# Optimization experiments

Measured on AMD Instinct MI355X. Metric: run time of the kernel, lower is better.

## Reference

```python
import jax, jax.numpy as jnp
import numpy as np

# dims (see shape_source)
B, S, DM, H, CIN, COUT, E = 4, 1024, 256, 8, 23, 256, 16
D2 = 2 * DM                                  # MoE dim = cat(attn_out, queries)
HE = int(D2 * 4 * 2 / 3)                     # geglu/expert hidden = 1365
CAP = max(4, min(S, int(S * 2.0 / E)))       # eval capacity_factor=2.0 -> 128
THRESH = 0.2                                 # threshold_eval for 2nd expert
BAL_COEF, Z_COEF = 0.01, 0.001


def _gelu(x):
    return jax.nn.gelu(x, approximate=False)  # torch nn.GELU default = erf


def _layernorm(x, g, b, eps=1e-5):
    m = x.mean(-1, keepdims=True)
    v = ((x - m) ** 2).mean(-1, keepdims=True)
    return (x - m) * jax.lax.rsqrt(v + eps) * g + b


def _rmsnorm(x, g):
    # st-moe RMSNorm: F.normalize(x) * sqrt(d) * gamma
    n = jnp.sqrt((x * x).sum(-1, keepdims=True))
    return x / jnp.maximum(n, 1e-12) * jnp.float32(np.sqrt(x.shape[-1])) * g


def _geglu_ff(x, g, w1, b1, mult, w2, b2):
    # st-moe Expert with prenorm=True: RMSNorm -> Linear -> GEGLU -> Linear
    h = _rmsnorm(x, g) @ w1 + b1
    a, gate = jnp.split(h, 2, axis=-1)
    return (_gelu(gate) * a * mult) @ w2 + b2


def _mha(q_in, k_in, v_in, wq, bq, wk, bk, wv, bv, wo, bo):
    b, sq, d = q_in.shape
    hd = d // H
    def heads(t):
        return t.reshape(b, -1, H, hd).transpose(0, 2, 1, 3)  # (b,H,s,hd)
    q = heads(q_in @ wq + bq)
    k = heads(k_in @ wk + bk)
    v = heads(v_in @ wv + bv)
    scale = jnp.float32(1.0 / np.sqrt(hd))
    att = jax.nn.softmax(jnp.einsum('bhqd,bhkd->bhqk', q, k) * scale, axis=-1)
    o = jnp.einsum('bhqk,bhkd->bhqd', att, v).transpose(0, 2, 1, 3).reshape(b, sq, d)
    return o @ wo + bo


def _moe(x, gate_w, ln_g, ln_b, w1, b1, w2, b2):
    # top-2 gating with threshold + capacity, dense dispatch/combine (eval semantics)
    logits = jnp.einsum('bnd,ed->bne', x, gate_w)
    raw = jax.nn.softmax(logits, axis=-1)
    gates2, idx2 = jax.lax.top_k(raw, 2)                       # (b,n,2)
    gates2 = gates2 / jnp.maximum(gates2.sum(-1, keepdims=True), 1e-9)
    g1, g2 = gates2[..., 0], gates2[..., 1]
    route2 = (g2 > THRESH).astype(x.dtype)
    oh1 = jax.nn.one_hot(idx2[..., 0], E, dtype=x.dtype)       # (b,n,e)
    oh2 = jax.nn.one_hot(idx2[..., 1], E, dtype=x.dtype) * route2[..., None]
    pos1 = jnp.cumsum(oh1, axis=1) - oh1                       # slot within expert
    pos2 = jnp.cumsum(oh2, axis=1) - oh2 + oh1.sum(axis=1, keepdims=True)
    keep1 = oh1 * (pos1 < CAP).astype(x.dtype)
    keep2 = oh2 * (pos2 < CAP).astype(x.dtype)
    capoh1 = jax.nn.one_hot(jnp.clip(pos1, 0, CAP - 1).astype(jnp.int32), CAP, dtype=x.dtype)
    capoh2 = jax.nn.one_hot(jnp.clip(pos2, 0, CAP - 1).astype(jnp.int32), CAP, dtype=x.dtype)
    combine = (g1[..., None, None] * keep1[..., None] * capoh1
               + g2[..., None, None] * keep2[..., None] * capoh2)  # (b,n,e,c)
    dispatch = (combine > 0).astype(x.dtype)
    xin = jnp.einsum('bnec,bnd->ebcd', dispatch, x)            # (e,b,c,d)
    # Expert_alt: LayerNorm -> Linear -> LeakyReLU -> Linear, vectorized over experts
    h = _layernorm(xin, ln_g[:, None, None, :], ln_b[:, None, None, :])
    h = jax.nn.leaky_relu(jnp.einsum('ebcd,edh->ebch', h, w1) + b1[:, None, None, :])
    h = jnp.einsum('ebch,ehd->ebcd', h, w2) + b2[:, None, None, :]
    out = jnp.einsum('bnec,ebcd->bnd', combine, h)
    balance = (raw.mean(axis=1) * oh1.mean(axis=1)).mean() * jnp.float32(E * E) * BAL_COEF
    z = (jax.nn.logsumexp(logits, axis=-1) ** 2).mean() * Z_COEF
    return out, balance + z, balance, z


def setup_inputs() -> dict:
    key = jax.random.key(0)
    ks = iter(jax.random.split(key, 64))
    f32 = jnp.float32
    def rn(shape, std=0.02):
        return jax.random.normal(next(ks), shape, dtype=f32) * std
    return {
        'K': jax.random.normal(next(ks), (B, S, 3), dtype=f32),
        'V': jax.random.normal(next(ks), (B, S, CIN), dtype=f32),
        'Q': jax.random.normal(next(ks), (B, S, 3), dtype=f32),
        'w_topo': rn((3, DM)), 'b_topo': jnp.zeros((DM,), f32),
        'w_val': rn((CIN, DM)), 'b_val': jnp.zeros((DM,), f32),
        'wq': rn((DM, DM)), 'bq': jnp.zeros((DM,), f32),
        'wk': rn((DM, DM)), 'bk': jnp.zeros((DM,), f32),
        'wv': rn((DM, DM)), 'bv': jnp.zeros((DM,), f32),
        'wo': rn((DM, DM)), 'bo': jnp.zeros((DM,), f32),
        'ffb_g': jnp.ones((D2,), f32), 'ffb_w1': rn((D2, 2 * HE)),
        'ffb_b1': jnp.zeros((2 * HE,), f32), 'ffb_mult': jnp.ones((HE,), f32),
        'ffb_w2': rn((HE, D2)), 'ffb_b2': jnp.zeros((D2,), f32),
        'prenorm_g': jnp.ones((D2,), f32),
        'gate_w': rn((E, D2)),
        'exp_ln_g': jnp.ones((E, D2), f32), 'exp_ln_b': jnp.zeros((E, D2), f32),
        'exp_w1': rn((E, D2, HE)), 'exp_b1': jnp.zeros((E, HE), f32),
        'exp_w2': rn((E, HE, D2)), 'exp_b2': jnp.zeros((E, D2), f32),
        'ffa_g': jnp.ones((D2,), f32), 'ffa_w1': rn((D2, 2 * HE)),
        'ffa_b1': jnp.zeros((2 * HE,), f32), 'ffa_mult': jnp.ones((HE,), f32),
        'ffa_w2': rn((HE, D2)), 'ffa_b2': jnp.zeros((D2,), f32),
        'w_out': rn((D2, COUT)), 'b_out': jnp.zeros((COUT,), f32),
    }


def reference(K, V, Q, w_topo, b_topo, w_val, b_val, wq, bq, wk, bk, wv, bv, wo, bo,
              ffb_g, ffb_w1, ffb_b1, ffb_mult, ffb_w2, ffb_b2, prenorm_g, gate_w,
              exp_ln_g, exp_ln_b, exp_w1, exp_b1, exp_w2, exp_b2,
              ffa_g, ffa_w1, ffa_b1, ffa_mult, ffa_w2, ffa_b2, w_out, b_out):
    sk = K.shape[1]
    topo = _gelu(jnp.concatenate([K, Q], axis=1) @ w_topo + b_topo)
    keys, queries = topo[:, :sk], topo[:, sk:]
    values = _gelu(V @ w_val + b_val)
    attn = _mha(queries, keys, values, wq, bq, wk, bk, wv, bv, wo, bo)
    x = jnp.concatenate([attn, queries], axis=-1)      # (B, S, D2)
    # SparseMoEBlock with add_ff_before/add_ff_after = True (STMoE_prenorm)
    x = _geglu_ff(x, ffb_g, ffb_w1, ffb_b1, ffb_mult, ffb_w2, ffb_b2) + x
    moe_out, total_aux, bal, z = _moe(_rmsnorm(x, prenorm_g), gate_w,
                                      exp_ln_g, exp_ln_b, exp_w1, exp_b1, exp_w2, exp_b2)
    x = moe_out + x
    x = _geglu_ff(x, ffa_g, ffa_w1, ffa_b1, ffa_mult, ffa_w2, ffa_b2) + x
    out = _gelu(x @ w_out + b_out)
    return out, total_aux, bal, z
```

## Files before the change

kernel.cpp:

```cpp
#include <hip/hip_runtime.h>
#include <hip/hip_bf16.h>
#include <math.h>

#define CAPN 128

typedef short short8 __attribute__((ext_vector_type(8)));
typedef short short4v __attribute__((ext_vector_type(4)));
typedef float f32x4 __attribute__((ext_vector_type(4)));

__device__ __forceinline__ float gelu_f(float x){
  return 0.5f*x*(1.0f+erff(x*0.7071067811865476f));
}
__device__ __forceinline__ void split2(float v, __hip_bfloat16& h, __hip_bfloat16& l){
  h = __float2bfloat16(v);
  l = __float2bfloat16(v - __bfloat162float(h));
}
__device__ __forceinline__ void split2s(float v, short& h, short& l){
  __hip_bfloat16 hh = __float2bfloat16(v);
  __hip_bfloat16 ll = __float2bfloat16(v - __bfloat162float(hh));
  h = *(short*)&hh; l = *(short*)&ll;
}

__global__ __launch_bounds__(256) void topo_kernel(
    const float* __restrict__ K, const float* __restrict__ Q,
    const float* __restrict__ w, const float* __restrict__ b,
    __hip_bfloat16* __restrict__ khi, __hip_bfloat16* __restrict__ klo,
    __hip_bfloat16* __restrict__ qhi, __hip_bfloat16* __restrict__ qlo,
    float* __restrict__ qf32)
{
  int idx = blockIdx.x*256 + threadIdx.x;
  int d = idx & 255;
  int r = idx >> 8;
  int bb = r >> 11;
  int n  = r & 2047;
  const float* src = (n < 1024) ? (K + ((bb<<10) + n)*3)
                                : (Q + ((bb<<10) + (n-1024))*3);
  float v = b[d] + src[0]*w[d] + src[1]*w[256+d] + src[2]*w[512+d];
  v = gelu_f(v);
  int off = (((bb<<10) + (n & 1023))<<8) + d;
  __hip_bfloat16 h, l; split2(v, h, l);
  if (n < 1024){ khi[off] = h; klo[off] = l; }
  else         { qhi[off] = h; qlo[off] = l; qf32[off] = v; }
}

__global__ __launch_bounds__(256) void values_kernel(
    const float* __restrict__ V, const float* __restrict__ w,
    const float* __restrict__ b,
    __hip_bfloat16* __restrict__ vhi, __hip_bfloat16* __restrict__ vlo)
{
  int idx = blockIdx.x*256 + threadIdx.x;
  int d = idx & 255; int r = idx >> 8;
  const float* src = V + r*23;
  float acc = b[d];
  #pragma unroll
  for (int c=0;c<23;c++) acc += src[c]*w[c*256+d];
  acc = gelu_f(acc);
  __hip_bfloat16 h, l; split2(acc, h, l);
  vhi[idx] = h; vlo[idx] = l;
}

#define SLP 40
__global__ __launch_bounds__(256) void sgemm_kernel(
    const __hip_bfloat16* __restrict__ Ah_, const __hip_bfloat16* __restrict__ Al_,
    int lda, long sA,
    const __hip_bfloat16* __restrict__ Wh_, const __hip_bfloat16* __restrict__ Wl_,
    int ldw, long sW,
    const float* __restrict__ bias, int nbias, int bsplit, int bsplitPad, long sB,
    const float* __restrict__ R, int ldr,
    float* __restrict__ C, int ldc, long sC,
    int K, int act,
    float* __restrict__ P, long pz, int splitK)
{
  int z = blockIdx.z / splitK;
  int kc = blockIdx.z - z*splitK;
  const short* Ah = (const short*)Ah_ + (long)z*sA;
  const short* Al = (const short*)Al_ + (long)z*sA;
  const short* Wh = (const short*)Wh_ + (long)z*sW;
  const short* Wl = (const short*)Wl_ + (long)z*sW;
  int bm = blockIdx.y*128, bn = blockIdx.x*128;
  int tid = threadIdx.x, lane = tid & 63, wave = tid >> 6;
  int wm = (wave & 1)*64, wn = (wave >> 1)*64;

  __shared__ short AsH[128*SLP], AsL[128*SLP], BsH[128*SLP], BsL[128*SLP];

  f32x4 acc[4][4];
  f32x4 zero4 = {0.f,0.f,0.f,0.f};
  #pragma unroll
  for (int i=0;i<4;i++)
    #pragma unroll
    for (int j=0;j<4;j++) acc[i][j] = zero4;

  int srow = tid >> 1, scol = (tid & 1)*16;
  int ml = lane & 15, q = lane >> 4;
  long abase = (long)(bm+srow)*lda + scol;
  long bbase = (long)(bn+srow)*ldw + scol;

  int Kc = K / splitK;
  int kbeg = kc * Kc, kend = kbeg + Kc;

  short8 ah0 = *(const short8*)&Ah[abase + kbeg];
  short8 ah1 = *(const short8*)&Ah[abase + kbeg + 8];
  short8 al0 = *(const short8*)&Al[abase + kbeg];
  short8 al1 = *(const short8*)&Al[abase + kbeg + 8];
  short8 bh0 = *(const short8*)&Wh[bbase + kbeg];
  short8 bh1 = *(const short8*)&Wh[bbase + kbeg + 8];
  short8 bl0 = *(const short8*)&Wl[bbase + kbeg];
  short8 bl1 = *(const short8*)&Wl[bbase + kbeg + 8];

  for (int k0 = kbeg; k0 < kend; k0 += 32){
    __syncthreads();
    *(short8*)&AsH[srow*SLP + scol]     = ah0;
    *(short8*)&AsH[srow*SLP + scol + 8] = ah1;
    *(short8*)&AsL[srow*SLP + scol]     = al0;
    *(short8*)&AsL[srow*SLP + scol + 8] = al1;
    *(short8*)&BsH[srow*SLP + scol]     = bh0;
    *(short8*)&BsH[srow*SLP + scol + 8] = bh1;
    *(short8*)&BsL[srow*SLP + scol]     = bl0;
    *(short8*)&BsL[srow*SLP + scol + 8] = bl1;
    __syncthreads();
    if (k0 + 32 < kend){
      long ab = abase + k0 + 32;
      long bb2 = bbase + k0 + 32;
      ah0 = *(const short8*)&Ah[ab];
      ah1 = *(const short8*)&Ah[ab + 8];
      al0 = *(const short8*)&Al[ab];
      al1 = *(const short8*)&Al[ab + 8];
      bh0 = *(const short8*)&Wh[bb2];
      bh1 = *(const short8*)&Wh[bb2 + 8];
      bl0 = *(const short8*)&Wl[bb2];
      bl1 = *(const short8*)&Wl[bb2 + 8];
    }
    short8 afh[4], afl[4], bfh[4], bfl[4];
    #pragma unroll
    for (int i=0;i<4;i++){
      afh[i] = *(const short8*)&AsH[(wm + 16*i + ml)*SLP + q*8];
      afl[i] = *(const short8*)&AsL[(wm + 16*i + ml)*SLP + q*8];
    }
    #pragma unroll
    for (int j=0;j<4;j++){
      bfh[j] = *(const short8*)&BsH[(wn + 16*j + ml)*SLP + q*8];
      bfl[j] = *(const short8*)&BsL[(wn + 16*j + ml)*SLP + q*8];
    }
    #pragma unroll
    for (int i=0;i<4;i++)
      #pragma unroll
      for (int j=0;j<4;j++){
        acc[i][j] = __builtin_amdgcn_mfma_f32_16x16x32_bf16(afh[i], bfh[j], acc[i][j], 0,0,0);
        acc[i][j] = __builtin_amdgcn_mfma_f32_16x16x32_bf16(afh[i], bfl[j], acc[i][j], 0,0,0);
        acc[i][j] = __builtin_amdgcn_mfma_f32_16x16x32_bf16(afl[i], bfh[j], acc[i][j], 0,0,0);
      }
  }

  if (P){
    float* Pb = P + (long)blockIdx.z * pz;
    #pragma unroll
    for (int i=0;i<4;i++)
      #pragma unroll
      for (int r=0;r<4;r++){
        int gm = bm + wm + 16*i + q*4 + r;
        #pragma unroll
        for (int j=0;j<4;j++){
          int gn = bn + wn + 16*j + ml;
          Pb[(long)gm*ldc + gn] = acc[i][j][r];
        }
      }
    return;
  }

  const float* biasz = bias ? bias + (long)z*sB : nullptr;
  long coff = (long)z*sC;
  #pragma unroll
  for (int i=0;i<4;i++){
    #pragma unroll
    for (int r=0;r<4;r++){
      int gm = bm + wm + 16*i + q*4 + r;
      #pragma unroll
      for (int j=0;j<4;j++){
        int gn = bn + wn + 16*j + ml;
        float v = acc[i][j][r];
        if (biasz){
          int bi;
          if (bsplit){
            if (gn < bsplit) bi = gn;
            else if (gn >= bsplitPad && gn < bsplitPad + (nbias - bsplit)) bi = gn - (bsplitPad - bsplit);
            else bi = -1;
          } else bi = (gn < nbias) ? gn : -1;
          if (bi >= 0) v += biasz[bi];
        }
        if (act == 1) v = gelu_f(v);
        if (R) v += R[(long)gm*ldr + gn];
        C[coff + (long)gm*ldc + gn] = v;
      }
    }
  }
}

#define LP 56
__global__ __launch_bounds__(256) void bgemm_kernel(
    const __hip_bfloat16* __restrict__ A, int lda, long sA,
    const __hip_bfloat16* __restrict__ WT, int ldw, long sW,
    const float* __restrict__ bias, int nbias, int bsplit, int bsplitPad, long sB,
    const float* __restrict__ R, int ldr, long sR,
    void* __restrict__ C, int ldc, long sC, int cIsBf16,
    int K, int act,
    float* __restrict__ P, long pz, int splitK)
{
  int z = blockIdx.z / splitK;
  int kc = blockIdx.z - z*splitK;
  const short* Ab = (const short*)A + (long)z*sA;
  const short* Bb = (const short*)WT + (long)z*sW;
  int bm = blockIdx.y*128, bn = blockIdx.x*128;
  int tid = threadIdx.x, lane = tid & 63, wave = tid >> 6;
  int wm = (wave & 1)*64, wn = (wave >> 1)*64;

  __shared__ short As[128*LP];
  __shared__ short Bs[128*LP];

  f32x4 acc[4][4];
  f32x4 zero4 = {0.f,0.f,0.f,0.f};
  #pragma unroll
  for (int i=0;i<4;i++)
    #pragma unroll
    for (int j=0;j<4;j++) acc[i][j] = zero4;

  int g0 = tid, g1 = tid + 256;
  int r0 = g0 >> 2, c0 = (g0 & 3) * 8;
  int r1 = g1 >> 2, c1 = (g1 & 3) * 8;
  int ml = lane & 15, q = lane >> 4;
  long a0base = (long)(bm+r0)*lda + c0;
  long a1base = (long)(bm+r1)*lda + c1;
  long b0base = (long)(bn+r0)*ldw + c0;
  long b1base = (long)(bn+r1)*ldw + c1;

  int Kc = K / splitK;
  int kbeg = kc * Kc, kend = kbeg + Kc;

  short8 av0 = *(const short8*)&Ab[a0base + kbeg];
  short8 av1 = *(const short8*)&Ab[a1base + kbeg];
  short8 bv0 = *(const short8*)&Bb[b0base + kbeg];
  short8 bv1 = *(const short8*)&Bb[b1base + kbeg];

  for (int k0 = kbeg; k0 < kend; k0 += 32){
    __syncthreads();
    *(short8*)&As[r0*LP + c0] = av0;
    *(short8*)&As[r1*LP + c1] = av1;
    *(short8*)&Bs[r0*LP + c0] = bv0;
    *(short8*)&Bs[r1*LP + c1] = bv1;
    __syncthreads();
    if (k0 + 32 < kend){
      av0 = *(const short8*)&Ab[a0base + k0 + 32];
      av1 = *(const short8*)&Ab[a1base + k0 + 32];
      bv0 = *(const short8*)&Bb[b0base + k0 + 32];
      bv1 = *(const short8*)&Bb[b1base + k0 + 32];
    }
    short8 af[4], bfv[4];
    #pragma unroll
    for (int i=0;i<4;i++) af[i]  = *(const short8*)&As[(wm + 16*i + ml)*LP + q*8];
    #pragma unroll
    for (int j=0;j<4;j++) bfv[j] = *(const short8*)&Bs[(wn + 16*j + ml)*LP + q*8];
    #pragma unroll
    for (int i=0;i<4;i++)
      #pragma unroll
      for (int j=0;j<4;j++)
        acc[i][j] = __builtin_amdgcn_mfma_f32_16x16x32_bf16(af[i], bfv[j], acc[i][j], 0,0,0);
  }

  if (P){
    float* Pb = P + (long)blockIdx.z * pz;
    #pragma unroll
    for (int i=0;i<4;i++)
      #pragma unroll
      for (int r=0;r<4;r++){
        int gm = bm + wm + 16*i + q*4 + r;
        #pragma unroll
        for (int j=0;j<4;j++){
          int gn = bn + wn + 16*j + ml;
          Pb[(long)gm*ldc + gn] = acc[i][j][r];
        }
      }
    return;
  }

  const float* biasz = bias ? bias + (long)z*sB : nullptr;
  const float* Rz = R ? R + (long)z*sR : nullptr;
  long coff = (long)z*sC;
  #pragma unroll
  for (int i=0;i<4;i++){
    #pragma unroll
    for (int r=0;r<4;r++){
      int gm = bm + wm + 16*i + q*4 + r;
      #pragma unroll
      for (int j=0;j<4;j++){
        int gn = bn + wn + 16*j + ml;
        float v = acc[i][j][r];
        if (biasz){
          int bi;
          if (bsplit){
            if (gn < bsplit) bi = gn;
            else if (gn >= bsplitPad && gn < bsplitPad + (nbias - bsplit)) bi = gn - (bsplitPad - bsplit);
            else bi = -1;
          } else bi = (gn < nbias) ? gn : -1;
          if (bi >= 0) v += biasz[bi];
        }
        if (act == 2) v = (v > 0.f) ? v : 0.01f*v;
        if (Rz) v += Rz[(long)gm*ldr + gn];
        if (cIsBf16) ((__hip_bfloat16*)C)[coff + (long)gm*ldc + gn] = __float2bfloat16(v);
        else         ((float*)C)[coff + (long)gm*ldc + gn] = v;
      }
    }
  }
}

__global__ __launch_bounds__(256) void reduce_kernel(
    const float* __restrict__ P, long zStride, int nsplit,
    const float* __restrict__ bias,
    const float* __restrict__ R, float* __restrict__ out,
    int Nmask, int logN, int ldOut, int act, long total)
{
  long idx = (long)blockIdx.x*256 + threadIdx.x;
  if (idx >= total) return;
  long zz = idx / zStride;
  long rem = idx - zz*zStride;
  const float* Pb = P + zz*(long)nsplit*zStride + rem;
  float v = 0.f;
  for (int k=0;k<nsplit;k++) v += Pb[(long)k*zStride];
// ... 49 lines not shown
  __shared__ float lds[64][65];
  #pragma unroll
  for (int i=0;i<16;i++){
    int e = tid + i*256;
    int kl = e >> 6, c = e & 63;
    int np = n0 + c;
    int ns;
    if (split){
      if (np < split) ns = np;
      else if (np >= splitPad && np < splitPad + (N - split)) ns = np - (splitPad - split);
      else ns = -1;
    } else ns = (np < N) ? np : -1;
    int k = k0 + kl;
    float v = (ns >= 0 && k < K) ? W[(long)k*N + ns] : 0.f;
    lds[kl][c] = v;
  }
  __syncthreads();
  #pragma unroll
  for (int i=0;i<16;i++){
    int e = tid + i*256;
    int nl = e >> 6, kl = e & 63;
    float v = lds[kl][nl];
    __hip_bfloat16 h, l; split2(v, h, l);
    long o = (long)(n0+nl)*Kpad + k0 + kl;
    outh[o] = h; outl[o] = l;
  }
}

__global__ void pack_bias_kernel(const float* bq, const float* bk, const float* bv, float* out){
  int i = blockIdx.x*256 + threadIdx.x;
  if (i < 256) out[i] = bq[i];
  else if (i < 512) out[i] = bk[i-256];
  else if (i < 768) out[i] = bv[i-512];
}

__global__ __launch_bounds__(256) void qksplit_kernel(
    const float* __restrict__ QP,
    __hip_bfloat16* __restrict__ qsh, __hip_bfloat16* __restrict__ qsl,
    __hip_bfloat16* __restrict__ ksh, __hip_bfloat16* __restrict__ ksl)
{
  int idx = blockIdx.x*256 + threadIdx.x;
  float qv = QP[idx] * 0.17677669529663687f;
  __hip_bfloat16 h, l;
  split2(qv, h, l); qsh[idx] = h; qsl[idx] = l;
  float kv = QP[1048576 + idx];
  split2(kv, h, l); ksh[idx] = h; ksl[idx] = l;
}

__global__ __launch_bounds__(256) void vtrans_kernel(
    const float* __restrict__ VP,
    __hip_bfloat16* __restrict__ vth, __hip_bfloat16* __restrict__ vtl)
{
  int bh = blockIdx.y, bb = bh >> 3, h = bh & 7;
  int s0 = blockIdx.x*64;
  int tid = threadIdx.x;
  __shared__ float t[64][33];
  #pragma unroll
  for (int p=0;p<8;p++){
    int sl = (tid>>5) + p*8;
    int d = tid & 31;
    t[sl][d] = VP[((bb<<10)+s0+sl)*256 + h*32 + d];
  }
  __syncthreads();
  #pragma unroll
  for (int p=0;p<8;p++){
    int dl = (tid>>6) + p*4;
    int s = tid & 63;
    float v = t[s][dl];
    __hip_bfloat16 hh, ll; split2(v, hh, ll);
    vth[(bh*32+dl)*1024 + s0 + s] = hh;
    vtl[(bh*32+dl)*1024 + s0 + s] = ll;
  }
}

#define KSP 40
__global__ __launch_bounds__(256) void attn_mfma_kernel(
    const __hip_bfloat16* __restrict__ qsh_, const __hip_bfloat16* __restrict__ qsl_,
    const __hip_bfloat16* __restrict__ ksh_, const __hip_bfloat16* __restrict__ ksl_,
    const __hip_bfloat16* __restrict__ vth_, const __hip_bfloat16* __restrict__ vtl_,
// ... 64 lines not shown
      split2s(p1, sh, sl2);
      Phw[ml*KSP + 16 + quad*4 + r] = sh;  Plw[ml*KSP + 16 + quad*4 + r] = sl2;
    }
    #pragma unroll
    for (int r=0;r<4;r++){
      float ar = __shfl(alpha, quad*4 + r, 16);
      O0[r] *= ar; O1[r] *= ar; Lacc[r] *= ar;
    }
    short8 pAh = *(const short8*)&Phw[ml*KSP + quad*8];
    short8 pAl = *(const short8*)&Plw[ml*KSP + quad*8];
    short8 vb0h = *(const short8*)&VhS[ml*KSP + quad*8];
    short8 vb0l = *(const short8*)&VlS[ml*KSP + quad*8];
    short8 vb1h = *(const short8*)&VhS[(16+ml)*KSP + quad*8];
    short8 vb1l = *(const short8*)&VlS[(16+ml)*KSP + quad*8];
    O0 = __builtin_amdgcn_mfma_f32_16x16x32_bf16(pAl, vb0h, O0, 0,0,0);
    O0 = __builtin_amdgcn_mfma_f32_16x16x32_bf16(pAh, vb0l, O0, 0,0,0);
    O0 = __builtin_amdgcn_mfma_f32_16x16x32_bf16(pAh, vb0h, O0, 0,0,0);
    O1 = __builtin_amdgcn_mfma_f32_16x16x32_bf16(pAl, vb1h, O1, 0,0,0);
    O1 = __builtin_amdgcn_mfma_f32_16x16x32_bf16(pAh, vb1l, O1, 0,0,0);
    O1 = __builtin_amdgcn_mfma_f32_16x16x32_bf16(pAh, vb1h, O1, 0,0,0);
    Lacc = __builtin_amdgcn_mfma_f32_16x16x32_bf16(pAh, ones, Lacc, 0,0,0);
    Lacc = __builtin_amdgcn_mfma_f32_16x16x32_bf16(pAl, ones, Lacc, 0,0,0);
  }
  #pragma unroll
  for (int r=0;r<4;r++){
    float inv = 1.f / Lacc[r];
    int row = (bb<<10) + q0 + quad*4 + r;
    __hip_bfloat16 hh, ll;
    split2(O0[r]*inv, hh, ll);
    aoh[row*256 + h*32 + ml] = hh;       aol[row*256 + h*32 + ml] = ll;
    split2(O1[r]*inv, hh, ll);
    aoh[row*256 + h*32 + 16 + ml] = hh;  aol[row*256 + h*32 + 16 + ml] = ll;
  }
}

__global__ __launch_bounds__(256) void concat_kernel(
    const float* __restrict__ queries, float* __restrict__ x)
{
  int idx = blockIdx.x*256 + threadIdx.x;
  int d = idx & 255; int r = idx >> 8;
  x[(r<<9) + 256 + d] = queries[idx];
}

__global__ __launch_bounds__(256) void rmsnorm_kernel(
    const float* __restrict__ x, const float* __restrict__ g, float* __restrict__ y)
{
  int r = blockIdx.x; int tid = threadIdx.x;
  float v0 = x[(r<<9) + tid];
  float v1 = x[(r<<9) + 256 + tid];
  float ss = v0*v0 + v1*v1;
  #pragma unroll
  for (int off=32; off>0; off>>=1) ss += __shfl_down(ss, off, 64);
  __shared__ float wsum[4];
  if ((tid & 63) == 0) wsum[tid>>6] = ss;
  __syncthreads();
  float tot = wsum[0]+wsum[1]+wsum[2]+wsum[3];
  float scale = 22.62741699796952f / fmaxf(sqrtf(tot), 1e-12f);
  y[(r<<9) + tid]       = v0*scale*g[tid];
  y[(r<<9) + 256 + tid] = v1*scale*g[256+tid];
}

__global__ __launch_bounds__(256) void rmsnorm_split_kernel(
    const float* __restrict__ x, const float* __restrict__ g,
    __hip_bfloat16* __restrict__ yh, __hip_bfloat16* __restrict__ yl)
{
  int r = blockIdx.x; int tid = threadIdx.x;
  float v0 = x[(r<<9) + tid];
  float v1 = x[(r<<9) + 256 + tid];
  float ss = v0*v0 + v1*v1;
  #pragma unroll
  for (int off=32; off>0; off>>=1) ss += __shfl_down(ss, off, 64);
  __shared__ float wsum[4];
  if ((tid & 63) == 0) wsum[tid>>6] = ss;
  __syncthreads();
// ... 275 lines not shown
  const float* gate_w = (const float*)d_in[22];
  const float* exp_ln_g=(const float*)d_in[23];
  const float* exp_ln_b=(const float*)d_in[24];
  const float* exp_w1 = (const float*)d_in[25];
  const float* exp_b1 = (const float*)d_in[26];
  const float* exp_w2 = (const float*)d_in[27];
  const float* exp_b2 = (const float*)d_in[28];
  const float* ffa_g  = (const float*)d_in[29];
  const float* ffa_w1 = (const float*)d_in[30];
  const float* ffa_b1 = (const float*)d_in[31];
  const float* ffa_mult=(const float*)d_in[32];
  const float* ffa_w2 = (const float*)d_in[33];
  const float* ffa_b2 = (const float*)d_in[34];
  const float* w_out  = (const float*)d_in[35];
  const float* b_out  = (const float*)d_in[36];
  float* dout = (float*)d_out;

  float* wsf = (float*)d_ws;
  int*   wsi = (int*)d_ws;

  const size_t A0 = 0;
  const size_t B0 = 11534336;
  const size_t OXA = 17301504;
  const size_t OXB = 19398656;
  const size_t OWP = 21495808;
  const size_t OMI = 21889024;

  __hip_bfloat16* qhi = (__hip_bfloat16*)(wsf + A0);
  __hip_bfloat16* khi = (__hip_bfloat16*)(wsf + A0 + 524288);
  __hip_bfloat16* vhi = (__hip_bfloat16*)(wsf + A0 + 1048576);
  __hip_bfloat16* qlo = (__hip_bfloat16*)(wsf + A0 + 1572864);
  __hip_bfloat16* klo = (__hip_bfloat16*)(wsf + A0 + 2097152);
  __hip_bfloat16* vlo = (__hip_bfloat16*)(wsf + A0 + 2621440);
  float* QP = wsf + A0 + 3145728;
  __hip_bfloat16* aohi = (__hip_bfloat16*)(wsf + A0 + 6291456);
  __hip_bfloat16* aolo = (__hip_bfloat16*)(wsf + A0 + 6815744);
  __hip_bfloat16* qsh = (__hip_bfloat16*)(wsf + A0);
  __hip_bfloat16* qsl = (__hip_bfloat16*)(wsf + A0 + 524288);
  __hip_bfloat16* ksh = (__hip_bfloat16*)(wsf + A0 + 1048576);
  __hip_bfloat16* ksl = (__hip_bfloat16*)(wsf + A0 + 1572864);
  __hip_bfloat16* vth = (__hip_bfloat16*)(wsf + A0 + 2097152);
  __hip_bfloat16* vtl = (__hip_bfloat16*)(wsf + A0 + 2621440);
  float* QF = wsf + B0 + 262144;
  float* Hb = wsf + A0;
  __hip_bfloat16* yh   = (__hip_bfloat16*)(wsf + B0);
  __hip_bfloat16* yl   = (__hip_bfloat16*)(wsf + B0 + 1048576);
  __hip_bfloat16* fw1h = (__hip_bfloat16*)(wsf + B0 + 2097152);
  __hip_bfloat16* fw1l = fw1h + 1441792;
  __hip_bfloat16* th   = (__hip_bfloat16*)(wsf + B0);
  __hip_bfloat16* tl   = (__hip_bfloat16*)(wsf + B0 + 2883584);
  __hip_bfloat16* fw2h = (__hip_bfloat16*)(wsf + A0);
  __hip_bfloat16* fw2l = fw2h + 720896;
  float* Pffb = wsf + A0 + 1048576;
  __hip_bfloat16* wte   = (__hip_bfloat16*)(wsf + A0);
  __hip_bfloat16* xin_bf= (__hip_bfloat16*)(wsf + A0 + 5767168);
  __hip_bfloat16* h1_bf = (__hip_bfloat16*)(wsf + A0 + 7864320);
  float* H2 = wsf + 13631488;
  float* YM = wsf + B0;
  __hip_bfloat16* y_bf = (__hip_bfloat16*)(wsf + A0);
  __hip_bfloat16* wf1  = (__hip_bfloat16*)(wsf + A0 + 1048576);
  __hip_bfloat16* h_bf = (__hip_bfloat16*)(wsf + A0 + 1769472);
  __hip_bfloat16* t_bf = (__hip_bfloat16*)(wsf + A0 + 7536640);
  __hip_bfloat16* wf2  = (__hip_bfloat16*)(wsf + A0 + 10420224);
  float* Pffa = wsf + B0;
  __hip_bfloat16* xah = (__hip_bfloat16*)(wsf + A0);
  __hip_bfloat16* xal = (__hip_bfloat16*)(wsf + A0 + 1048576);
  float* Pout = wsf + A0 + 2097152;
  __hip_bfloat16* wp = (__hip_bfloat16*)(wsf + OWP);
  __hip_bfloat16* wqh = wp;            __hip_bfloat16* wkh = wp + 65536;
  __hip_bfloat16* wvh = wp + 131072;   __hip_bfloat16* wql = wp + 196608;
  __hip_bfloat16* wkl = wp + 262144;   __hip_bfloat16* wvl = wp + 327680;
  __hip_bfloat16* woh = wp + 393216;   __hip_bfloat16* wol = wp + 458752;
  __hip_bfloat16* wouth = wp + 524288; __hip_bfloat16* woutl = wp + 655360;

  int* idx1 = wsi + OMI + 0;
  int* idx2 = wsi + OMI + 4096;
  int* route= wsi + OMI + 8192;
  int* ts1  = wsi + OMI + 12288;
  int* ts2  = wsi + OMI + 16384;
  int* slot_token = wsi + OMI + 20480;
  int* count1     = wsi + OMI + 28672;
  float* gg1      = wsf + OMI + 28864;
  float* gg2      = wsf + OMI + 32960;
  float* bias_qkv = wsf + OMI + 37056;
  float* rawp     = wsf + OMI + 37824;
  float* lse2     = wsf + OMI + 103360;

  convT2_kernel<<<dim3(4,4),  256, 0, stream>>>(wq, 256, 256, wqh, wql, 256, 256, 0, 0);
  convT2_kernel<<<dim3(4,4),  256, 0, stream>>>(wk, 256, 256, wkh, wkl, 256, 256, 0, 0);
  convT2_kernel<<<dim3(4,4),  256, 0, stream>>>(wv, 256, 256, wvh, wvl, 256, 256, 0, 0);
  convT2_kernel<<<dim3(4,4),  256, 0, stream>>>(wo, 256, 256, woh, wol, 256, 256, 0, 0);
  convT2_kernel<<<dim3(4,8),  256, 0, stream>>>(w_out, 256, 512, wouth, woutl, 256, 512, 0, 0);
  convT2_kernel<<<dim3(44,8), 256, 0, stream>>>(ffb_w1, 2730, 512, fw1h, fw1l, 2816, 512, 1365, 1408);
  pack_bias_kernel<<<3, 256, 0, stream>>>(bq, bk, bv, bias_qkv);

  topo_kernel<<<8192, 256, 0, stream>>>(K_in, Q_in, w_topo, b_topo, khi, klo, qhi, qlo, QF);
  values_kernel<<<4096, 256, 0, stream>>>(V_in, w_val, b_val, vhi, vlo);

  sgemm_kernel<<<dim3(2,32,3), 256, 0, stream>>>(
      qhi, qlo, 256, 1048576, wqh, wql, 256, 65536,
      bias_qkv, 256, 0, 0, 256, nullptr, 0, QP, 256, 1048576, 256, 0,
      nullptr, 0, 1);

  qksplit_kernel<<<4096, 256, 0, stream>>>(QP, qsh, qsl, ksh, ksl);
  vtrans_kernel<<<dim3(16,32), 256, 0, stream>>>(QP + 2097152, vth, vtl);
  attn_mfma_kernel<<<dim3(16,32), 256, 0, stream>>>(qsh, qsl, ksh, ksl, vth, vtl, aohi, aolo);

  sgemm_kernel<<<dim3(2,32,1), 256, 0, stream>>>(
      aohi, aolo, 256, 0, woh, wol, 256, 0,
      bo, 256, 0, 0, 0, nullptr, 0, wsf+OXA, 512, 0, 256, 0,
      nullptr, 0, 1);
  concat_kernel<<<4096, 256, 0, stream>>>(QF, wsf+OXA);

  rmsnorm_split_kernel<<<4096, 256, 0, stream>>>(wsf+OXA, ffb_g, yh, yl);
  sgemm_kernel<<<dim3(22,32,1), 256, 0, stream>>>(
      yh, yl, 512, 0, fw1h, fw1l, 512, 0,
      ffb_b1, 2730, 1365, 1408, 0, nullptr, 0, Hb, 2816, 0, 512, 0,
      nullptr, 0, 1);
  glu_split_kernel<<<22528, 256, 0, stream>>>(Hb, ffb_mult, th, tl);
  convT2_kernel<<<dim3(8,22), 256, 0, stream>>>(ffb_w2, 512, 1365, fw2h, fw2l, 512, 1408, 0, 0);
  sgemm_kernel<<<dim3(4,32,4), 256, 0, stream>>>(
      th, tl, 1408, 0, fw2h, fw2l, 1408, 0,
      nullptr, 0, 0, 0, 0, nullptr, 0, nullptr, 512, 0, 1408, 0,
      Pffb, 2097152, 4);
  reduce_kernel<<<8192, 256, 0, stream>>>(
      Pffb, 2097152, 4, ffb_b2, wsf+OXA, wsf+OXB, 511, 9, 512, 0, 2097152);

  rmsnorm_kernel<<<4096, 256, 0, stream>>>(wsf+OXB, prenorm_g, YM);
  gating_kernel<<<4096, 256, 0, stream>>>(YM, gate_w, idx1, idx2, route, gg1, gg2, rawp, lse2);
  scan_kernel<<<64, 256, 0, stream>>>(idx1, idx2, route, ts1, ts2, slot_token, count1);
  gather_ln_kernel<<<8192, 256, 0, stream>>>(YM, slot_token, exp_ln_g, exp_ln_b, xin_bf);
  convT_kernel<<<dim3(22, 8, 16), 256, 0, stream>>>(exp_w1, 1365, 512, (long)512*1365,
                                                    wte, 1408, 512, (long)1408*512, 0, 0);
  bgemm_kernel<<<dim3(11,4,16), 256, 0, stream>>>(
      xin_bf, 512, (long)512*512, wte, 512, (long)1408*512,
      exp_b1, 1365, 0, 0, 1365, nullptr, 0, 0,
      h1_bf, 1408, (long)512*1408, 1, 512, 2,
      nullptr, 0, 1);
  convT_kernel<<<dim3(8, 22, 16), 256, 0, stream>>>(exp_w2, 512, 1365, (long)1365*512,
                                                    wte, 512, 1408, (long)512*1408, 0, 0);
  bgemm_kernel<<<dim3(4,4,16), 256, 0, stream>>>(
      h1_bf, 1408, (long)512*1408, wte, 1408, (long)512*1408,
      exp_b2, 512, 0, 0, 512, nullptr, 0, 0,
      H2, 512, (long)512*512, 0, 1408, 0,
      nullptr, 0, 1);
  combine_kernel<<<8192, 256, 0, stream>>>(wsf+OXB, H2, ts1, ts2, gg1, gg2);
  aux_kernel<<<1, 256, 0, stream>>>(rawp, lse2, count1, dout + 4096*256);

  rmsnorm_bf_kernel<<<4096, 256, 0, stream>>>(wsf+OXB, ffa_g, y_bf);
  convT_kernel<<<dim3(44, 8, 1), 256, 0, stream>>>(ffa_w1, 2730, 512, 0,
                                                   wf1, 2816, 512, 0, 1365, 1408);
  bgemm_kernel<<<dim3(22,32,1), 256, 0, stream>>>(
      y_bf, 512, 0, wf1, 512, 0,
      ffa_b1, 2730, 1365, 1408, 0, nullptr, 0, 0,
      h_bf, 2816, 0, 1, 512, 0,
      nullptr, 0, 1);
  glu_bf_kernel<<<22528, 256, 0, stream>>>(h_bf, ffa_mult, t_bf);
  convT_kernel<<<dim3(8, 22, 1), 256, 0, stream>>>(ffa_w2, 512, 1365, 0,
                                                   wf2, 512, 1408, 0, 0, 0);
  bgemm_kernel<<<dim3(4,32,2), 256, 0, stream>>>(
      t_bf, 1408, 0, wf2, 1408, 0,
      nullptr, 0, 0, 0, 0, nullptr, 0, 0,
      nullptr, 512, 0, 0, 1408, 0,
      Pffa, 2097152, 2);
  reduce_kernel<<<8192, 256, 0, stream>>>(
      Pffa, 2097152, 2, ffa_b2, wsf+OXB, wsf+OXA, 511, 9, 512, 0, 2097152);

  split32_kernel<<<8192, 256, 0, stream>>>(wsf+OXA, xah, xal);
  sgemm_kernel<<<dim3(2,32,4), 256, 0, stream>>>(
      xah, xal, 512, 0, wouth, woutl, 512, 0,
      nullptr, 0, 0, 0, 0, nullptr, 0, nullptr, 256, 0, 512, 0,
      Pout, 1048576, 4);
  reduce_kernel<<<4096, 256, 0, stream>>>(
      Pout, 1048576, 4, b_out, nullptr, dout, 255, 8, 256, 1, 1048576);
}
```

Baseline: 804.8 us.

## Halve GEMM N-tile to 64 and fuse QK split and concat into producers

Both split-bf16 and plain bf16 GEMM kernels shrink their N tile from 128 to 64, with per-wave 64x32 sub-tiles and doubled grid widths, to raise block count and occupancy on the small GEMMs. The QKV projection epilogue now scales Q and writes hi/lo bf16 splits for Q and K directly, which removes the separate qksplit kernel. The topo kernel writes the queries straight into the concatenated x buffer, which removes the concat kernel. The smaller tiles lower per-block operand reuse and add more global loads per FLOP.

New measurement: 808.9 us. About the same (+0.5%).

```diff
diff --git a/kernel.cpp b/kernel.cpp
--- a/kernel.cpp
+++ b/kernel.cpp
@@ -26,7 +26,7 @@
     const float* __restrict__ w, const float* __restrict__ b,
     __hip_bfloat16* __restrict__ khi, __hip_bfloat16* __restrict__ klo,
     __hip_bfloat16* __restrict__ qhi, __hip_bfloat16* __restrict__ qlo,
-    float* __restrict__ qf32)
+    float* __restrict__ xa)
 {
   int idx = blockIdx.x*256 + threadIdx.x;
   int d = idx & 255;
@@ -37,10 +37,13 @@
                                 : (Q + ((bb<<10) + (n-1024))*3);
   float v = b[d] + src[0]*w[d] + src[1]*w[256+d] + src[2]*w[512+d];
   v = gelu_f(v);
-  int off = (((bb<<10) + (n & 1023))<<8) + d;
+  int tok = (bb<<10) + (n & 1023);
   __hip_bfloat16 h, l; split2(v, h, l);
-  if (n < 1024){ khi[off] = h; klo[off] = l; }
-  else         { qhi[off] = h; qlo[off] = l; qf32[off] = v; }
+  if (n < 1024){ khi[(tok<<8)+d] = h; klo[(tok<<8)+d] = l; }
+  else {
+    qhi[(tok<<8)+d] = h; qlo[(tok<<8)+d] = l;
+    xa[(tok<<9) + 256 + d] = v;
+  }
 }
 
 __global__ __launch_bounds__(256) void values_kernel(
@@ -69,7 +72,9 @@
     const float* __restrict__ R, int ldr,
     float* __restrict__ C, int ldc, long sC,
     int K, int act,
-    float* __restrict__ P, long pz, int splitK)
+    float* __restrict__ P, long pz, int splitK,
+    __hip_bfloat16* __restrict__ APh, __hip_bfloat16* __restrict__ APl,
+    long APz, int attnPrep)
 {
   int z = blockIdx.z / splitK;
   int kc = blockIdx.z - z*splitK;
@@ -77,23 +82,22 @@
   const short* Al = (const short*)Al_ + (long)z*sA;
   const short* Wh = (const short*)Wh_ + (long)z*sW;
   const short* Wl = (const short*)Wl_ + (long)z*sW;
-  int bm = blockIdx.y*128, bn = blockIdx.x*128;
+  int bm = blockIdx.y*128, bn = blockIdx.x*64;
   int tid = threadIdx.x, lane = tid & 63, wave = tid >> 6;
-  int wm = (wave & 1)*64, wn = (wave >> 1)*64;
-
-  __shared__ short AsH[128*SLP], AsL[128*SLP], BsH[128*SLP], BsL[128*SLP];
-
-  f32x4 acc[4][4];
+  int wm = (wave & 1)*64, wn = (wave >> 1)*32;
+
+  __shared__ short AsH[128*SLP], AsL[128*SLP], BsH[64*SLP], BsL[64*SLP];
+
+  f32x4 acc[4][2];
   f32x4 zero4 = {0.f,0.f,0.f,0.f};
   #pragma unroll
-  for (int i=0;i<4;i++)
-    #pragma unroll
-    for (int j=0;j<4;j++) acc[i][j] = zero4;
-
-  int srow = tid >> 1, scol = (tid & 1)*16;
+  for (int i=0;i<4;i++){ acc[i][0] = zero4; acc[i][1] = zero4; }
+
+  int arow = tid >> 1, acol = (tid & 1)*16;
+  int brow = tid >> 2, bcol = (tid & 3)*8;
   int ml = lane & 15, q = lane >> 4;
-  long abase = (long)(bm+srow)*lda + scol;
-  long bbase = (long)(bn+srow)*ldw + scol;
+  long abase = (long)(bm+arow)*lda + acol;
+  long bbase = (long)(bn+brow)*ldw + bcol;
 
   int Kc = K / splitK;
   int kbeg = kc * Kc, kend = kbeg + Kc;
@@ -103,20 +107,16 @@
   short8 al0 = *(const short8*)&Al[abase + kbeg];
   short8 al1 = *(const short8*)&Al[abase + kbeg + 8];
   short8 bh0 = *(const short8*)&Wh[bbase + kbeg];
-  short8 bh1 = *(const short8*)&Wh[bbase + kbeg + 8];
   short8 bl0 = *(const short8*)&Wl[bbase + kbeg];
-  short8 bl1 = *(const short8*)&Wl[bbase + kbeg + 8];
 
   for (int k0 = kbeg; k0 < kend; k0 += 32){
     __syncthreads();
-    *(short8*)&AsH[srow*SLP + scol]     = ah0;
-    *(short8*)&AsH[srow*SLP + scol + 8] = ah1;
-    *(short8*)&AsL[srow*SLP + scol]     = al0;
-    *(short8*)&AsL[srow*SLP + scol + 8] = al1;
-    *(short8*)&BsH[srow*SLP + scol]     = bh0;
-    *(short8*)&BsH[srow*SLP + scol + 8] = bh1;
-    *(short8*)&BsL[srow*SLP + scol]     = bl0;
-    *(short8*)&BsL[srow*SLP + scol + 8] = bl1;
+    *(short8*)&AsH[arow*SLP + acol]     = ah0;
+    *(short8*)&AsH[arow*SLP + acol + 8] = ah1;
+    *(short8*)&AsL[arow*SLP + acol]     = al0;
+    *(short8*)&AsL[arow*SLP + acol + 8] = al1;
+    *(short8*)&BsH[brow*SLP + bcol]     = bh0;
+    *(short8*)&BsL[brow*SLP + bcol]     = bl0;
     __syncthreads();
     if (k0 + 32 < kend){
       long ab = abase + k0 + 32;
@@ -126,25 +126,23 @@
       al0 = *(const short8*)&Al[ab];
       al1 = *(const short8*)&Al[ab + 8];
       bh0 = *(const short8*)&Wh[bb2];
-      bh1 = *(const short8*)&Wh[bb2 + 8];
       bl0 = *(const short8*)&Wl[bb2];
-      bl1 = *(const short8*)&Wl[bb2 + 8];
     }
-    short8 afh[4], afl[4], bfh[4], bfl[4];
+    short8 afh[4], afl[4], bfh[2], bfl[2];
     #pragma unroll
     for (int i=0;i<4;i++){
       afh[i] = *(const short8*)&AsH[(wm + 16*i + ml)*SLP + q*8];
       afl[i] = *(const short8*)&AsL[(wm + 16*i + ml)*SLP + q*8];
     }
     #pragma unroll
-    for (int j=0;j<4;j++){
+    for (int j=0;j<2;j++){
       bfh[j] = *(const short8*)&BsH[(wn + 16*j + ml)*SLP + q*8];
       bfl[j] = *(const short8*)&BsL[(wn + 16*j + ml)*SLP + q*8];
     }
     #pragma unroll
     for (int i=0;i<4;i++)
       #pragma unroll
-      for (int j=0;j<4;j++){
+      for (int j=0;j<2;j++){
         acc[i][j] = __builtin_amdgcn_mfma_f32_16x16x32_bf16(afh[i], bfh[j], acc[i][j], 0,0,0);
         acc[i][j] = __builtin_amdgcn_mfma_f32_16x16x32_bf16(afh[i], bfl[j], acc[i][j], 0,0,0);
         acc[i][j] = __builtin_amdgcn_mfma_f32_16x16x32_bf16(afl[i], bfh[j], acc[i][j], 0,0,0);
@@ -159,7 +157,7 @@
       for (int r=0;r<4;r++){
         int gm = bm + wm + 16*i + q*4 + r;
         #pragma unroll
-        for (int j=0;j<4;j++){
+        for (int j=0;j<2;j++){
           int gn = bn + wn + 16*j + ml;
           Pb[(long)gm*ldc + gn] = acc[i][j][r];
         }
@@ -175,7 +173,7 @@
     for (int r=0;r<4;r++){
       int gm = bm + wm + 16*i + q*4 + r;
       #pragma unroll
-      for (int j=0;j<4;j++){
+      for (int j=0;j<2;j++){
         int gn = bn + wn + 16*j + ml;
         float v = acc[i][j][r];
         if (biasz){
@@ -187,6 +185,17 @@
           } else bi = (gn < nbias) ? gn : -1;
           if (bi >= 0) v += biasz[bi];
         }
+        if (attnPrep){
+          if (z < 2){
+            if (z == 0) v *= 0.17677669529663687f;
+            __hip_bfloat16 hh, ll; split2(v, hh, ll);
+            APh[(long)z*APz + (long)gm*256 + gn] = hh;
+            APl[(long)z*APz + (long)gm*256 + gn] = ll;
+          } else {
+            C[(long)gm*ldc + gn] = v;
+          }
+          continue;
+        }
         if (act == 1) v = gelu_f(v);
         if (R) v += R[(long)gm*ldr + gn];
         C[coff + (long)gm*ldc + gn] = v;
@@ -195,7 +204,7 @@
   }
 }
 
-#define LP 56
+#define LP 40
 __global__ __launch_bounds__(256) void bgemm_kernel(
     const __hip_bfloat16* __restrict__ A, int lda, long sA,
     const __hip_bfloat16* __restrict__ WT, int ldw, long sW,
@@ -209,59 +218,51 @@
   int kc = blockIdx.z - z*splitK;
   const short* Ab = (const short*)A + (long)z*sA;
   const short* Bb = (const short*)WT + (long)z*sW;
-  int bm = blockIdx.y*128, bn = blockIdx.x*128;
+  int bm = blockIdx.y*128, bn = blockIdx.x*64;
   int tid = threadIdx.x, lane = tid & 63, wave = tid >> 6;
-  int wm = (wave & 1)*64, wn = (wave >> 1)*64;
+  int wm = (wave & 1)*64, wn = (wave >> 1)*32;
 
   __shared__ short As[128*LP];
-  __shared__ short Bs[128*LP];
-
-  f32x4 acc[4][4];
+  __shared__ short Bs[64*LP];
+
+  f32x4 acc[4][2];
   f32x4 zero4 = {0.f,0.f,0.f,0.f};
   #pragma unroll
-  for (int i=0;i<4;i++)
-    #pragma unroll
-    for (int j=0;j<4;j++) acc[i][j] = zero4;
-
-  int g0 = tid, g1 = tid + 256;
-  int r0 = g0 >> 2, c0 = (g0 & 3) * 8;
-  int r1 = g1 >> 2, c1 = (g1 & 3) * 8;
+  for (int i=0;i<4;i++){ acc[i][0] = zero4; acc[i][1] = zero4; }
+
+  int arow = tid >> 1, acol = (tid & 1)*16;
+  int brow = tid >> 2, bcol = (tid & 3)*8;
   int ml = lane & 15, q = lane >> 4;
-  long a0base = (long)(bm+r0)*lda + c0;
-  long a1base = (long)(bm+r1)*lda + c1;
-  long b0base = (long)(bn+r0)*ldw + c0;
-  long b1base = (long)(bn+r1)*ldw + c1;
+  long abase = (long)(bm+arow)*lda + acol;
+  long bbase = (long)(bn+brow)*ldw + bcol;
 
   int Kc = K / splitK;
   int kbeg = kc * Kc, kend = kbeg + Kc;
 
-  short8 av0 = *(const short8*)&Ab[a0base + kbeg];
-  short8 av1 = *(const short8*)&Ab[a1base + kbeg];
-  short8 bv0 = *(const short8*)&Bb[b0base + kbeg];
-  short8 bv1 = *(const short8*)&Bb[b1base + kbeg];
+  short8 av0 = *(const short8*)&Ab[abase + kbeg];
+  short8 av1 = *(const short8*)&Ab[abase + kbeg + 8];
+  short8 bv0 = *(const short8*)&Bb[bbase + kbeg];
 
   for (int k0 = kbeg; k0 < kend; k0 += 32){
     __syncthreads();
-    *(short8*)&As[r0*LP + c0] = av0;
-    *(short8*)&As[r1*LP + c1] = av1;
-    *(short8*)&Bs[r0*LP + c0] = bv0;
-    *(short8*)&Bs[r1*LP + c1] = bv1;
+    *(short8*)&As[arow*LP + acol]     = av0;
+    *(short8*)&As[arow*LP + acol + 8] = av1;
+    *(short8*)&Bs[brow*LP + bcol]     = bv0;
     __syncthreads();
     if (k0 + 32 < kend){
-      av0 = *(const short8*)&Ab[a0base + k0 + 32];
-      av1 = *(const short8*)&Ab[a1base + k0 + 32];
-      bv0 = *(const short8*)&Bb[b0base + k0 + 32];
-      bv1 = *(const short8*)&Bb[b1base + k0 + 32];
+      av0 = *(const short8*)&Ab[abase + k0 + 32];
+      av1 = *(const short8*)&Ab[abase + k0 + 40];
+      bv0 = *(const short8*)&Bb[bbase + k0 + 32];
     }
-    short8 af[4], bfv[4];
+    short8 af[4], bfv[2];
     #pragma unroll
     for (int i=0;i<4;i++) af[i]  = *(const short8*)&As[(wm + 16*i + ml)*LP + q*8];
     #pragma unroll
-    for (int j=0;j<4;j++) bfv[j] = *(const short8*)&Bs[(wn + 16*j + ml)*LP + q*8];
+    for (int j=0;j<2;j++) bfv[j] = *(const short8*)&Bs[(wn + 16*j + ml)*LP + q*8];
     #pragma unroll
     for (int i=0;i<4;i++)
       #pragma unroll
-      for (int j=0;j<4;j++)
+      for (int j=0;j<2;j++)
         acc[i][j] = __builtin_amdgcn_mfma_f32_16x16x32_bf16(af[i], bfv[j], acc[i][j], 0,0,0);
   }
 
@@ -273,7 +274,7 @@
       for (int r=0;r<4;r++){
         int gm = bm + wm + 16*i + q*4 + r;
         #pragma unroll
-        for (int j=0;j<4;j++){
+        for (int j=0;j<2;j++){
           int gn = bn + wn + 16*j + ml;
           Pb[(long)gm*ldc + gn] = acc[i][j][r];
         }
@@ -290,7 +291,7 @@
     for (int r=0;r<4;r++){
       int gm = bm + wm + 16*i + q*4 + r;
       #pragma unroll
-      for (int j=0;j<4;j++){
+      for (int j=0;j<2;j++){
         int gn = bn + wn + 16*j + ml;
         float v = acc[i][j][r];
         if (biasz){
@@ -406,19 +407,6 @@
   if (i < 256) out[i] = bq[i];
   else if (i < 512) out[i] = bk[i-256];
   else if (i < 768) out[i] = bv[i-512];
-}
-
-__global__ __launch_bounds__(256) void qksplit_kernel(
-    const float* __restrict__ QP,
-    __hip_bfloat16* __restrict__ qsh, __hip_bfloat16* __restrict__ qsl,
-    __hip_bfloat16* __restrict__ ksh, __hip_bfloat16* __restrict__ ksl)
-{
-  int idx = blockIdx.x*256 + threadIdx.x;
-  float qv = QP[idx] * 0.17677669529663687f;
-  __hip_bfloat16 h, l;
-  split2(qv, h, l); qsh[idx] = h; qsl[idx] = l;
-  float kv = QP[1048576 + idx];
-  split2(kv, h, l); ksh[idx] = h; ksl[idx] = l;
 }
 
 __global__ __launch_bounds__(256) void vtrans_kernel(
@@ -549,14 +537,6 @@
     split2(O1[r]*inv, hh, ll);
     aoh[row*256 + h*32 + 16 + ml] = hh;  aol[row*256 + h*32 + 16 + ml] = ll;
   }
-}
-
-__global__ __launch_bounds__(256) void concat_kernel(
-    const float* __restrict__ queries, float* __restrict__ x)
-{
-  int idx = blockIdx.x*256 + threadIdx.x;
-  int d = idx & 255; int r = idx >> 8;
-  x[(r<<9) + 256 + d] = queries[idx];
 }
 
 __global__ __launch_bounds__(256) void rmsnorm_kernel(
@@ -898,16 +878,13 @@
   __hip_bfloat16* qlo = (__hip_bfloat16*)(wsf + A0 + 1572864);
   __hip_bfloat16* klo = (__hip_bfloat16*)(wsf + A0 + 2097152);
   __hip_bfloat16* vlo = (__hip_bfloat16*)(wsf + A0 + 2621440);
-  float* QP = wsf + A0 + 3145728;
+  __hip_bfloat16* qsh2 = (__hip_bfloat16*)(wsf + A0 + 3145728);
+  __hip_bfloat16* qsl2 = (__hip_bfloat16*)(wsf + A0 + 3670016);
+  float* Vf32 = wsf + A0 + 5242880;
+  __hip_bfloat16* vth = (__hip_bfloat16*)(wsf + A0 + 2097152);
+  __hip_bfloat16* vtl = (__hip_bfloat16*)(wsf + A0 + 2621440);
   __hip_bfloat16* aohi = (__hip_bfloat16*)(wsf + A0 + 6291456);
   __hip_bfloat16* aolo = (__hip_bfloat16*)(wsf + A0 + 6815744);
-  __hip_bfloat16* qsh = (__hip_bfloat16*)(wsf + A0);
-  __hip_bfloat16* qsl = (__hip_bfloat16*)(wsf + A0 + 524288);
-  __hip_bfloat16* ksh = (__hip_bfloat16*)(wsf + A0 + 1048576);
-  __hip_bfloat16* ksl = (__hip_bfloat16*)(wsf + A0 + 1572864);
-  __hip_bfloat16* vth = (__hip_bfloat16*)(wsf + A0 + 2097152);
-  __hip_bfloat16* vtl = (__hip_bfloat16*)(wsf + A0 + 2621440);
-  float* QF = wsf + B0 + 262144;
   float* Hb = wsf + A0;
   __hip_bfloat16* yh   = (__hip_bfloat16*)(wsf + B0);
   __hip_bfloat16* yl   = (__hip_bfloat16*)(wsf + B0 + 1048576);
@@ -960,35 +937,35 @@
   convT2_kernel<<<dim3(44,8), 256, 0, stream>>>(ffb_w1, 2730, 512, fw1h, fw1l, 2816, 512, 1365, 1408);
   pack_bias_kernel<<<3, 256, 0, stream>>>(bq, bk, bv, bias_qkv);
 
-  topo_kernel<<<8192, 256, 0, stream>>>(K_in, Q_in, w_topo, b_topo, khi, klo, qhi, qlo, QF);
+  topo_kernel<<<8192, 256, 0, stream>>>(K_in, Q_in, w_topo, b_topo, khi, klo, qhi, qlo, wsf+OXA);
   values_kernel<<<4096, 256, 0, stream>>>(V_in, w_val, b_val, vhi, vlo);
 
-  sgemm_kernel<<<dim3(2,32,3), 256, 0, stream>>>(
+  sgemm_kernel<<<dim3(4,32,3), 256, 0, stream>>>(
       qhi, qlo, 256, 1048576, wqh, wql, 256, 65536,
-      bias_qkv, 256, 0, 0, 256, nullptr, 0, QP, 256, 1048576, 256, 0,
-      nullptr, 0, 1);
-
-  qksplit_kernel<<<4096, 256, 0, stream>>>(QP, qsh, qsl, ksh, ksl);
-  vtrans_kernel<<<dim3(16,32), 256, 0, stream>>>(QP + 2097152, vth, vtl);
-  attn_mfma_kernel<<<dim3(16,32), 256, 0, stream>>>(qsh, qsl, ksh, ksl, vth, vtl, aohi, aolo);
-
-  sgemm_kernel<<<dim3(2,32,1), 256, 0, stream>>>(
+      bias_qkv, 256, 0, 0, 256, nullptr, 0, Vf32, 256, 0, 256, 0,
+      nullptr, 0, 1,
+      qsh2, qsl2, 2097152, 1);
+
+  vtrans_kernel<<<dim3(16,32), 256, 0, stream>>>(Vf32, vth, vtl);
+  attn_mfma_kernel<<<dim3(16,32), 256, 0, stream>>>(
+      qsh2, qsl2, qsh2 + 2097152, qsl2 + 2097152, vth, vtl, aohi, aolo);
+
+  sgemm_kernel<<<dim3(4,32,1), 256, 0, stream>>>(
       aohi, aolo, 256, 0, woh, wol, 256, 0,
       bo, 256, 0, 0, 0, nullptr, 0, wsf+OXA, 512, 0, 256, 0,
-      nullptr, 0, 1);
-  concat_kernel<<<4096, 256, 0, stream>>>(QF, wsf+OXA);
+      nullptr, 0, 1, nullptr, nullptr, 0, 0);
 
   rmsnorm_split_kernel<<<4096, 256, 0, stream>>>(wsf+OXA, ffb_g, yh, yl);
-  sgemm_kernel<<<dim3(22,32,1), 256, 0, stream>>>(
+  sgemm_kernel<<<dim3(44,32,1), 256, 0, stream>>>(
       yh, yl, 512, 0, fw1h, fw1l, 512, 0,
       ffb_b1, 2730, 1365, 1408, 0, nullptr, 0, Hb, 2816, 0, 512, 0,
-      nullptr, 0, 1);
+      nullptr, 0, 1, nullptr, nullptr, 0, 0);
   glu_split_kernel<<<22528, 256, 0, stream>>>(Hb, ffb_mult, th, tl);
   convT2_kernel<<<dim3(8,22), 256, 0, stream>>>(ffb_w2, 512, 1365, fw2h, fw2l, 512, 1408, 0, 0);
-  sgemm_kernel<<<dim3(4,32,4), 256, 0, stream>>>(
+  sgemm_kernel<<<dim3(8,32,4), 256, 0, stream>>>(
       th, tl, 1408, 0, fw2h, fw2l, 1408, 0,
       nullptr, 0, 0, 0, 0, nullptr, 0, nullptr, 512, 0, 1408, 0,
-      Pffb, 2097152, 4);
+      Pffb, 2097152, 4, nullptr, nullptr, 0, 0);
   reduce_kernel<<<8192, 256, 0, stream>>>(
       Pffb, 2097152, 4, ffb_b2, wsf+OXA, wsf+OXB, 511, 9, 512, 0, 2097152);
 
@@ -998,14 +975,14 @@
   gather_ln_kernel<<<8192, 256, 0, stream>>>(YM, slot_token, exp_ln_g, exp_ln_b, xin_bf);
   convT_kernel<<<dim3(22, 8, 16), 256, 0, stream>>>(exp_w1, 1365, 512, (long)512*1365,
                                                     wte, 1408, 512, (long)1408*512, 0, 0);
-  bgemm_kernel<<<dim3(11,4,16), 256, 0, stream>>>(
+  bgemm_kernel<<<dim3(22,4,16), 256, 0, stream>>>(
       xin_bf, 512, (long)512*512, wte, 512, (long)1408*512,
       exp_b1, 1365, 0, 0, 1365, nullptr, 0, 0,
       h1_bf, 1408, (long)512*1408, 1, 512, 2,
       nullptr, 0, 1);
   convT_kernel<<<dim3(8, 22, 16), 256, 0, stream>>>(exp_w2, 512, 1365, (long)1365*512,
                                                     wte, 512, 1408, (long)512*1408, 0, 0);
-  bgemm_kernel<<<dim3(4,4,16), 256, 0, stream>>>(
+  bgemm_kernel<<<dim3(8,4,16), 256, 0, stream>>>(
       h1_bf, 1408, (long)512*1408, wte, 1408, (long)512*1408,
       exp_b2, 512, 0, 0, 512, nullptr, 0, 0,
       H2, 512, (long)512*512, 0, 1408, 0,
@@ -1016,7 +993,7 @@
   rmsnorm_bf_kernel<<<4096, 256, 0, stream>>>(wsf+OXB, ffa_g, y_bf);
   convT_kernel<<<dim3(44, 8, 1), 256, 0, stream>>>(ffa_w1, 2730, 512, 0,
                                                    wf1, 2816, 512, 0, 1365, 1408);
-  bgemm_kernel<<<dim3(22,32,1), 256, 0, stream>>>(
+  bgemm_kernel<<<dim3(44,32,1), 256, 0, stream>>>(
       y_bf, 512, 0, wf1, 512, 0,
       ffa_b1, 2730, 1365, 1408, 0, nullptr, 0, 0,
       h_bf, 2816, 0, 1, 512, 0,
@@ -1024,7 +1001,7 @@
   glu_bf_kernel<<<22528, 256, 0, stream>>>(h_bf, ffa_mult, t_bf);
   convT_kernel<<<dim3(8, 22, 1), 256, 0, stream>>>(ffa_w2, 512, 1365, 0,
                                                    wf2, 512, 1408, 0, 0, 0);
-  bgemm_kernel<<<dim3(4,32,2), 256, 0, stream>>>(
+  bgemm_kernel<<<dim3(8,32,2), 256, 0, stream>>>(
       t_bf, 1408, 0, wf2, 1408, 0,
       nullptr, 0, 0, 0, 0, nullptr, 0, 0,
       nullptr, 512, 0, 0, 1408, 0,
@@ -1033,10 +1010,10 @@
       Pffa, 2097152, 2, ffa_b2, wsf+OXB, wsf+OXA, 511, 9, 512, 0, 2097152);
 
   split32_kernel<<<8192, 256, 0, stream>>>(wsf+OXA, xah, xal);
-  sgemm_kernel<<<dim3(2,32,4), 256, 0, stream>>>(
+  sgemm_kernel<<<dim3(4,32,4), 256, 0, stream>>>(
       xah, xal, 512, 0, wouth, woutl, 512, 0,
       nullptr, 0, 0, 0, 0, nullptr, 0, nullptr, 256, 0, 512, 0,
-      Pout, 1048576, 4);
+      Pout, 1048576, 4, nullptr, nullptr, 0, 0);
   reduce_kernel<<<4096, 256, 0, stream>>>(
       Pout, 1048576, 4, b_out, nullptr, dout, 255, 8, 256, 1, 1048576);
 }
```
